# Optimization experiments

Hardware: AMD Instinct MI355X
Metric: run time of the kernel (lower is better)

## Reference

```python
import jax, jax.numpy as jnp
import numpy as np

N = 100000   # nodes
E = 1600000  # edges
IN, HID, OUT = 128, 256, 64


def _glorot(key, shape):
    fan_in, fan_out = shape[1], shape[0]
    lim = (6.0 / (fan_in + fan_out)) ** 0.5
    return jax.random.uniform(key, shape, jnp.float32, -lim, lim)


def setup_inputs() -> dict:
    key = jax.random.key(0)
    ks = jax.random.split(key, 8)
    x = jax.random.normal(ks[0], (N, IN), jnp.float32)
    edge_index = jax.random.randint(ks[1], (2, E), 0, N, jnp.int64)
    # SAGEConv params: lin_l (neighbor path, has bias), lin_r (root path, no bias)
    return {
        "x": x,
        "edge_index": edge_index,
        "W1_l": _glorot(ks[2], (HID, IN)),
        "b1": jnp.zeros((HID,), jnp.float32),
        "W1_r": _glorot(ks[3], (HID, IN)),
        "W2_l": _glorot(ks[4], (OUT, HID)),
        "b2": jnp.zeros((OUT,), jnp.float32),
        "W2_r": _glorot(ks[5], (OUT, HID)),
    }


def _sage_conv(x, src, dst, W_l, b, W_r):
    # mean aggregation of neighbor features at destination nodes
    msg = x[src]                                             # [E, d] gather
    agg = jax.ops.segment_sum(msg, dst, num_segments=N)      # [N, d]
    cnt = jax.ops.segment_sum(jnp.ones((src.shape[0],), jnp.float32), dst,
                              num_segments=N)                # [N]
    mean = agg / jnp.maximum(cnt, 1.0)[:, None]
    return mean @ W_l.T + b + x @ W_r.T


def reference(x, edge_index, W1_l, b1, W1_r, W2_l, b2, W2_r):
    src, dst = edge_index[0], edge_index[1]
    h = jax.nn.relu(_sage_conv(x, src, dst, W1_l, b1, W1_r))
    # dropout is identity in eval mode
    return _sage_conv(h, src, dst, W2_l, b2, W2_r)
```

## Files before the change

### kernel.cpp

```cpp
#include <hip/hip_runtime.h>
#include <hip/hip_bf16.h>

#define NNODE 100000
#define NEDGE 1600000
#define NBBLK 512
#define CHUNK (NEDGE / NBBLK)
#define NBUCK ((NNODE + 511) >> 9)
#define XB ((NNODE * 32 + 255) / 256)
#define WB 384

typedef __attribute__((ext_vector_type(8))) short bf16x8;
typedef __attribute__((ext_vector_type(4))) float f32x4;
typedef __attribute__((ext_vector_type(2))) float f32x2;

__device__ __forceinline__ unsigned short f2bf(float f){
  unsigned u = __float_as_uint(f);
  u += 0x7fffu + ((u >> 16) & 1u);
  return (unsigned short)(u >> 16);
}
__device__ __forceinline__ unsigned pk2(float a, float b){
  return (unsigned)f2bf(a) | ((unsigned)f2bf(b) << 16);
}
__device__ __forceinline__ float bflo(unsigned v){ return __uint_as_float(v << 16); }
__device__ __forceinline__ float bfhi(unsigned v){ return __uint_as_float(v & 0xffff0000u); }

__global__ __launch_bounds__(256) void k_xh(const float* __restrict__ x,
                                            unsigned* __restrict__ A1u,
                                            unsigned* __restrict__ x8u,
                                            const int* __restrict__ dst,
                                            unsigned* __restrict__ gh,
                                            const float* __restrict__ W1l,
                                            const float* __restrict__ W1r,
                                            const float* __restrict__ W2l,
                                            const float* __restrict__ W2r,
                                            unsigned short* __restrict__ Bwt1,
                                            unsigned short* __restrict__ Bwt2){
  int bid = blockIdx.x;
  if (bid < NBBLK){
    __shared__ unsigned h[NBUCK];
    for (int t = threadIdx.x; t < NBUCK; t += 256) h[t] = 0;
    __syncthreads();
    int base = bid * CHUNK;
    for (int j = threadIdx.x; j < CHUNK; j += 256)
      atomicAdd(&h[dst[base + j] >> 9], 1u);
    __syncthreads();
    for (int t = threadIdx.x; t < NBUCK; t += 256) gh[bid * NBUCK + t] = h[t];
    return;
  }
  if (bid < NBBLK + XB){
    int i = (bid - NBBLK) * 256 + threadIdx.x;
    if (i >= NNODE * 32) return;
    float4 v = ((const float4*)x)[i];
    int e = i * 4;
    int row = e >> 7, c = e & 127;
    unsigned* d = A1u + (size_t)row * 128 + 64 + (c >> 1);
    d[0] = pk2(v.x, v.y);
    d[1] = pk2(v.z, v.w);
    unsigned p = (unsigned)__builtin_amdgcn_cvt_pk_fp8_f32(v.x, v.y, 0, false);
    p = (unsigned)__builtin_amdgcn_cvt_pk_fp8_f32(v.z, v.w, (int)p, true);
    x8u[(size_t)row * 32 + (c >> 2)] = p;
    return;
  }
  int i = (bid - NBBLK - XB) * 256 + threadIdx.x;
  if (i < 256 * 256){
    int n = i >> 8, k = i & 255;
    float v = (k < 128) ? W1l[n * 128 + k] : W1r[n * 128 + (k - 128)];
    Bwt1[i] = f2bf(v);
  } else if (i < 256 * 256 + 128 * 256){
    int i2 = i - 256 * 256;
    int n = i2 >> 8, k = i2 & 255;
    float v = (n < 64) ? W2l[n * 256 + k] : W2r[(n - 64) * 256 + k];
    Bwt2[i2] = f2bf(v);
  }
}

__global__ __launch_bounds__(512) void k_scan512(const unsigned* __restrict__ gh,
                                                 unsigned* __restrict__ gbase,
                                                 unsigned* __restrict__ btot){
  int b = blockIdx.x, t = threadIdx.x;
  int lane = t & 63, wv = t >> 6;
  unsigned v = gh[t * NBUCK + b];
  unsigned s = v;
  #pragma unroll
  for (int off = 1; off < 64; off <<= 1){
    unsigned u = __shfl_up(s, off, 64);
    if (lane >= off) s += u;
  }
  __shared__ unsigned wsum[8];
  if (lane == 63) wsum[wv] = s;
  __syncthreads();
  unsigned woff = 0;
  for (int w = 0; w < wv; ++w) woff += wsum[w];
  gbase[t * NBUCK + b] = woff + s - v;
  if (t == 511) btot[b] = woff + s;
}

__global__ __launch_bounds__(256) void k_binscat(const int* __restrict__ src,
                                                 const int* __restrict__ dst,
                                                 const unsigned* __restrict__ gbase,
                                                 const unsigned* __restrict__ btot,
                                                 unsigned* __restrict__ pairs){
  __shared__ unsigned sb[256];
  __shared__ unsigned cur[NBUCK];
  int t = threadIdx.x;
  unsigned v = (t < NBUCK) ? btot[t] : 0u;
  sb[t] = v;
  __syncthreads();
  #pragma unroll
  for (int off = 1; off < 256; off <<= 1){
    unsigned u = (t >= off) ? sb[t - off] : 0u;
    __syncthreads();
    sb[t] += u;
    __syncthreads();
  }
  if (t < NBUCK) cur[t] = (sb[t] - v) + gbase[blockIdx.x * NBUCK + t];
  __syncthreads();
  int base = blockIdx.x * CHUNK;
  for (int j = t; j < CHUNK; j += 256){
    int s = src[base + j], d = dst[base + j];
    unsigned p = atomicAdd(&cur[d >> 9], 1u);
    pairs[p] = ((unsigned)s << 9) | (unsigned)(d & 511);
  }
}

__global__ __launch_bounds__(512) void k_buildcsr(const unsigned* __restrict__ btot,
                                                  const unsigned* __restrict__ pairs,
                                                  unsigned* __restrict__ rowptr,
                                                  unsigned* __restrict__ col){
  __shared__ unsigned sb[256];
  __shared__ unsigned hist[512];
  __shared__ unsigned wsum[8];
  __shared__ unsigned se0, se1;
  const int b = blockIdx.x, tid = threadIdx.x;
  const int lane = tid & 63, wv = tid >> 6;
  if (tid < 256){
    unsigned v = (tid < NBUCK) ? btot[tid] : 0u;
    sb[tid] = v;
  }
  __syncthreads();
  #pragma unroll
  for (int off = 1; off < 256; off <<= 1){
    unsigned u = 0;
    if (tid < 256 && tid >= off) u = sb[tid - off];
    __syncthreads();
    if (tid < 256) sb[tid] += u;
    __syncthreads();
  }
  if (tid == 0){
    se1 = sb[b];
    se0 = sb[b] - btot[b];
    if (b == 0) rowptr[NNODE] = NEDGE;
  }
  hist[tid] = 0;
  __syncthreads();
  const unsigned e0 = se0, e1 = se1;
  const int nb0 = b << 9;
  for (unsigned j = e0 + tid; j < e1; j += 512)
    atomicAdd(&hist[pairs[j] & 511u], 1u);
  __syncthreads();
  unsigned v = hist[tid];
  unsigned s = v;
  #pragma unroll
  for (int off = 1; off < 64; off <<= 1){
    unsigned u = __shfl_up(s, off, 64);
    if (lane >= off) s += u;
  }
  if (lane == 63) wsum[wv] = s;
  __syncthreads();
  unsigned woff = 0;
  for (int w = 0; w < wv; ++w) woff += wsum[w];
  unsigned gpos = e0 + woff + s - v;
  if (nb0 + tid < NNODE) rowptr[nb0 + tid] = gpos;
  __syncthreads();
  hist[tid] = gpos;
  __syncthreads();
  for (unsigned j = e0 + tid; j < e1; j += 512){
    unsigned e = pairs[j];
    unsigned p = atomicAdd(&hist[e & 511u], 1u);
    col[p] = e >> 9;
  }
}

__global__ __launch_bounds__(256) void k_agg1(const unsigned* __restrict__ rowptr,
                                              const unsigned* __restrict__ col,
                                              const unsigned* __restrict__ x8u,
                                              unsigned* __restrict__ A1u){
  int gw = (blockIdx.x * 256 + threadIdx.x) >> 6;
  int lane = threadIdx.x & 63;
  if (gw >= NNODE) return;
  unsigned s0 = rowptr[gw], s1 = rowptr[gw + 1];
  const int sel = lane >> 4, u = lane & 15;
  const uint2* x82 = (const uint2*)x8u;
  float a0=0.f,a1=0.f,a2=0.f,a3=0.f,a4=0.f,a5=0.f,a6=0.f,a7=0.f;
  f32x2 p;
  unsigned j = s0;
  for (; j + 15 < s1; j += 16){
    unsigned ca = col[j + sel], cb = col[j + 4 + sel];
    unsigned cc = col[j + 8 + sel], cd = col[j + 12 + sel];
    uint2 va = x82[(size_t)ca * 16 + u];
    uint2 vb = x82[(size_t)cb * 16 + u];
    uint2 vc = x82[(size_t)cc * 16 + u];
    uint2 vd = x82[(size_t)cd * 16 + u];
    p = __builtin_amdgcn_cvt_pk_f32_fp8((int)va.x, false); a0+=p.x; a1+=p.y;
    p = __builtin_amdgcn_cvt_pk_f32_fp8((int)va.x, true ); a2+=p.x; a3+=p.y;
    p = __builtin_amdgcn_cvt_pk_f32_fp8((int)va.y, false); a4+=p.x; a5+=p.y;
    p = __builtin_amdgcn_cvt_pk_f32_fp8((int)va.y, true ); a6+=p.x; a7+=p.y;
    p = __builtin_amdgcn_cvt_pk_f32_fp8((int)vb.x, false); a0+=p.x; a1+=p.y;
    p = __builtin_amdgcn_cvt_pk_f32_fp8((int)vb.x, true ); a2+=p.x; a3+=p.y;
    p = __builtin_amdgcn_cvt_pk_f32_fp8((int)vb.y, false); a4+=p.x; a5+=p.y;
    p = __builtin_amdgcn_cvt_pk_f32_fp8((int)vb.y, true ); a6+=p.x; a7+=p.y;
    p = __builtin_amdgcn_cvt_pk_f32_fp8((int)vc.x, false); a0+=p.x; a1+=p.y;
    p = __builtin_amdgcn_cvt_pk_f32_fp8((int)vc.x, true ); a2+=p.x; a3+=p.y;
    p = __builtin_amdgcn_cvt_pk_f32_fp8((int)vc.y, false); a4+=p.x; a5+=p.y;
    p = __builtin_amdgcn_cvt_pk_f32_fp8((int)vc.y, true ); a6+=p.x; a7+=p.y;
    p = __builtin_amdgcn_cvt_pk_f32_fp8((int)vd.x, false); a0+=p.x; a1+=p.y;
    p = __builtin_amdgcn_cvt_pk_f32_fp8((int)vd.x, true ); a2+=p.x; a3+=p.y;
    p = __builtin_amdgcn_cvt_pk_f32_fp8((int)vd.y, false); a4+=p.x; a5+=p.y;
    p = __builtin_amdgcn_cvt_pk_f32_fp8((int)vd.y, true ); a6+=p.x; a7+=p.y;
  }
  for (; j + 3 < s1; j += 4){
    unsigned ca = col[j + sel];
    uint2 va = x82[(size_t)ca * 16 + u];
    p = __builtin_amdgcn_cvt_pk_f32_fp8((int)va.x, false); a0+=p.x; a1+=p.y;
    p = __builtin_amdgcn_cvt_pk_f32_fp8((int)va.x, true ); a2+=p.x; a3+=p.y;
    p = __builtin_amdgcn_cvt_pk_f32_fp8((int)va.y, false); a4+=p.x; a5+=p.y;
    p = __builtin_amdgcn_cvt_pk_f32_fp8((int)va.y, true ); a6+=p.x; a7+=p.y;
  }
  int rem = (int)(s1 - j);
  if (sel < rem){
    unsigned ca = col[j + sel];
    uint2 va = x82[(size_t)ca * 16 + u];
    p = __builtin_amdgcn_cvt_pk_f32_fp8((int)va.x, false); a0+=p.x; a1+=p.y;
    p = __builtin_amdgcn_cvt_pk_f32_fp8((int)va.x, true ); a2+=p.x; a3+=p.y;
    p = __builtin_amdgcn_cvt_pk_f32_fp8((int)va.y, false); a4+=p.x; a5+=p.y;
    p = __builtin_amdgcn_cvt_pk_f32_fp8((int)va.y, true ); a6+=p.x; a7+=p.y;
  }
  a0 += __shfl_xor(a0, 16, 64); a1 += __shfl_xor(a1, 16, 64);
  a2 += __shfl_xor(a2, 16, 64); a3 += __shfl_xor(a3, 16, 64);
  a4 += __shfl_xor(a4, 16, 64); a5 += __shfl_xor(a5, 16, 64);
  a6 += __shfl_xor(a6, 16, 64); a7 += __shfl_xor(a7, 16, 64);
  a0 += __shfl_xor(a0, 32, 64); a1 += __shfl_xor(a1, 32, 64);
  a2 += __shfl_xor(a2, 32, 64); a3 += __shfl_xor(a3, 32, 64);
  a4 += __shfl_xor(a4, 32, 64); a5 += __shfl_xor(a5, 32, 64);
  a6 += __shfl_xor(a6, 32, 64); a7 += __shfl_xor(a7, 32, 64);
  if (lane < 16){
    float inv = 1.f / fmaxf((float)(s1 - s0), 1.f);
    uint4 w;
    w.x = pk2(a0 * inv, a1 * inv);
    w.y = pk2(a2 * inv, a3 * inv);
    w.z = pk2(a4 * inv, a5 * inv);
    w.w = pk2(a6 * inv, a7 * inv);
    *(uint4*)(A1u + (size_t)gw * 128 + 4 * lane) = w;
  }
}

template<int BN, bool RELU, bool BIAS, int MODE>
__global__ __launch_bounds__(512) void k_gemm(const unsigned short* __restrict__ A,
                                              const unsigned short* __restrict__ B,
                                              const float* __restrict__ bias,
                                              unsigned short* __restrict__ C,
                                              unsigned char* __restrict__ z8,
                                              unsigned short* __restrict__ r16,
                                              int nrows){
  constexpr int NF = BN / 64;
  __shared__ unsigned short a_t[128 * 64];
  __shared__ unsigned short b_t[BN * 64];
  const int tid = threadIdx.x, wave = tid >> 6, lane = tid & 63;
  const int wr = wave >> 2, wc = wave & 3;
  const int row0 = blockIdx.x * 128;
  char* ab = (char*)a_t;
  char* bb = (char*)b_t;

  f32x4 acc[4][NF];
  #pragma unroll
  for (int m = 0; m < 4; ++m)
    #pragma unroll
    for (int n = 0; n < NF; ++n)
      acc[m][n] = (f32x4){0.f, 0.f, 0.f, 0.f};

  for (int kt = 0; kt < 4; ++kt){
    {
      int r = tid >> 2;
      int gr = row0 + r; if (gr > nrows - 1) gr = nrows - 1;
      const uint4* s4 = (const uint4*)(A + (size_t)gr * 256 + kt * 64);
      int c0 = (tid & 3) * 2;
      uint4 v0 = s4[c0], v1 = s4[c0 + 1];
      *(uint4*)(ab + r * 128 + ((c0 * 16) ^ ((r & 7) << 4))) = v0;
      *(uint4*)(ab + r * 128 + (((c0 + 1) * 16) ^ ((r & 7) << 4))) = v1;
    }
    {
      constexpr int CPT = BN / 64;
      #pragma unroll
      for (int c = 0; c < CPT; ++c){
        int gc = tid * CPT + c;
        int n = gc >> 3, ck = gc & 7;
        uint4 v = ((const uint4*)(B + (size_t)n * 256 + kt * 64))[ck];
        *(uint4*)(bb + n * 128 + ((ck * 16) ^ ((n & 7) << 4))) = v;
      }
    }
    __syncthreads();
    #pragma unroll
    for (int kk = 0; kk < 2; ++kk){
      int k2 = (kk * 32 + ((lane >> 4) * 8)) * 2;
      bf16x8 af[4];
      #pragma unroll
      for (int m = 0; m < 4; ++m){
        int rr = wr * 64 + m * 16 + (lane & 15);
        af[m] = *(const bf16x8*)(ab + rr * 128 + (k2 ^ ((rr & 7) << 4)));
      }
      #pragma unroll
      for (int n = 0; n < NF; ++n){
        int cc = wc * (16 * NF) + n * 16 + (lane & 15);
        bf16x8 bfv = *(const bf16x8*)(bb + cc * 128 + (k2 ^ ((cc & 7) << 4)));
        #pragma unroll
        for (int m = 0; m < 4; ++m)
          acc[m][n] = __builtin_amdgcn_mfma_f32_16x16x32_bf16(af[m], bfv, acc[m][n], 0, 0, 0);
      }
    }
    __syncthreads();
  }
  #pragma unroll
  for (int m = 0; m < 4; ++m){
    int rbase = row0 + wr * 64 + m * 16 + ((lane >> 4) << 2);
    #pragma unroll
    for (int r = 0; r < 4; ++r){
      if (rbase + r < nrows){
        #pragma unroll
        for (int n = 0; n < NF; ++n){
          int cc = wc * (16 * NF) + n * 16 + (lane & 15);
          float v = acc[m][n][r];
          if (BIAS) v += bias[cc];
          if (RELU) v = fmaxf(v, 0.f);
          if (MODE == 0){
            C[(size_t)(rbase + r) * BN + cc] = f2bf(v);
          } else {
            if (cc < 64)
              z8[(size_t)(rbase + r) * 64 + cc] =
                (unsigned char)__builtin_amdgcn_cvt_pk_fp8_f32(v, v, 0, false);
            else
              r16[(size_t)(rbase + r) * 64 + (cc - 64)] = f2bf(v);
          }
        }
      }
    }
  }
}

__global__ __launch_bounds__(256) void k_agg2(const unsigned* __restrict__ rowptr,
                                              const unsigned* __restrict__ col,
                                              const unsigned* __restrict__ z8u,
                                              const unsigned* __restrict__ r16u,
                                              const float* __restrict__ b2,
                                              float* __restrict__ out){
  int gw = (blockIdx.x * 256 + threadIdx.x) >> 6;
  int lane = threadIdx.x & 63;
  if (gw >= NNODE) return;
  unsigned s0 = rowptr[gw], s1 = rowptr[gw + 1];
  const int sel = lane >> 4, u = lane & 15;
  float a0=0.f,a1=0.f,a2=0.f,a3=0.f;
  f32x2 p;
  unsigned j = s0;
  for (; j + 15 < s1; j += 16){
    unsigned ca = col[j + sel], cb = col[j + 4 + sel];
    unsigned cc = col[j + 8 + sel], cd = col[j + 12 + sel];
    unsigned va = z8u[(size_t)ca * 16 + u];
    unsigned vb = z8u[(size_t)cb * 16 + u];
    unsigned vc = z8u[(size_t)cc * 16 + u];
    unsigned vd = z8u[(size_t)cd * 16 + u];
    p = __builtin_amdgcn_cvt_pk_f32_fp8((int)va, false); a0+=p.x; a1+=p.y;
    p = __builtin_amdgcn_cvt_pk_f32_fp8((int)va, true ); a2+=p.x; a3+=p.y;
    p = __builtin_amdgcn_cvt_pk_f32_fp8((int)vb, false); a0+=p.x; a1+=p.y;
    p = __builtin_amdgcn_cvt_pk_f32_fp8((int)vb, true ); a2+=p.x; a3+=p.y;
    p = __builtin_amdgcn_cvt_pk_f32_fp8((int)vc, false); a0+=p.x; a1+=p.y;
    p = __builtin_amdgcn_cvt_pk_f32_fp8((int)vc, true ); a2+=p.x; a3+=p.y;
    p = __builtin_amdgcn_cvt_pk_f32_fp8((int)vd, false); a0+=p.x; a1+=p.y;
    p = __builtin_amdgcn_cvt_pk_f32_fp8((int)vd, true ); a2+=p.x; a3+=p.y;
  }
  for (; j + 3 < s1; j += 4){
    unsigned ca = col[j + sel];
    unsigned va = z8u[(size_t)ca * 16 + u];
    p = __builtin_amdgcn_cvt_pk_f32_fp8((int)va, false); a0+=p.x; a1+=p.y;
    p = __builtin_amdgcn_cvt_pk_f32_fp8((int)va, true ); a2+=p.x; a3+=p.y;
  }
  int rem = (int)(s1 - j);
  if (sel < rem){
    unsigned ca = col[j + sel];
    unsigned va = z8u[(size_t)ca * 16 + u];
    p = __builtin_amdgcn_cvt_pk_f32_fp8((int)va, false); a0+=p.x; a1+=p.y;
    p = __builtin_amdgcn_cvt_pk_f32_fp8((int)va, true ); a2+=p.x; a3+=p.y;
  }
  a0 += __shfl_xor(a0, 16, 64); a1 += __shfl_xor(a1, 16, 64);
  a2 += __shfl_xor(a2, 16, 64); a3 += __shfl_xor(a3, 16, 64);
  a0 += __shfl_xor(a0, 32, 64); a1 += __shfl_xor(a1, 32, 64);
  a2 += __shfl_xor(a2, 32, 64); a3 += __shfl_xor(a3, 32, 64);
  if (lane < 16){
    float inv = 1.f / fmaxf((float)(s1 - s0), 1.f);
    uint2 rv = ((const uint2*)(r16u + (size_t)gw * 32))[lane];
    float4 bv = ((const float4*)b2)[lane];
    float4 res;
    res.x = a0 * inv + bflo(rv.x) + bv.x;
    res.y = a1 * inv + bfhi(rv.x) + bv.y;
    res.z = a2 * inv + bflo(rv.y) + bv.z;
    res.w = a3 * inv + bfhi(rv.y) + bv.w;
    ((float4*)out)[(size_t)gw * 16 + lane] = res;
  }
}

extern "C" void kernel_launch(void* const* d_in, const int* in_sizes, int n_in,
                              void* d_out, int out_size, void* d_ws, size_t ws_size,
                              hipStream_t stream) {
  const float* x   = (const float*)d_in[0];
  const int*   ei  = (const int*)d_in[1];
  const float* W1l = (const float*)d_in[2];
  const float* b1  = (const float*)d_in[3];
  const float* W1r = (const float*)d_in[4];
  const float* W2l = (const float*)d_in[5];
  const float* b2  = (const float*)d_in[6];
  const float* W2r = (const float*)d_in[7];
  float* out = (float*)d_out;

  char* ws = (char*)d_ws;
  size_t off = 0;
  auto alloc = [&](size_t bytes) -> void* {
    void* p = ws + off;
    off = (off + bytes + 255) & ~(size_t)255;
    return p;
  };
  unsigned* rowptr = (unsigned*)alloc((size_t)(NNODE + 1) * 4);
  unsigned* col    = (unsigned*)alloc((size_t)NEDGE * 4);
  unsigned* pairs  = (unsigned*)alloc((size_t)NEDGE * 4);
  unsigned* gh     = (unsigned*)alloc((size_t)NBBLK * NBUCK * 4);
  unsigned* gbase  = (unsigned*)alloc((size_t)NBBLK * NBUCK * 4);
  unsigned* btot   = (unsigned*)alloc((size_t)NBUCK * 4);
  unsigned short* A1   = (unsigned short*)alloc((size_t)NNODE * 256 * 2);
  unsigned short* h    = (unsigned short*)alloc((size_t)NNODE * 256 * 2);
  unsigned short* r16  = (unsigned short*)alloc((size_t)NNODE * 64 * 2);
  unsigned* x8u        = (unsigned*)alloc((size_t)NNODE * 32 * 4);
  unsigned char* z8    = (unsigned char*)alloc((size_t)NNODE * 64);
  unsigned short* Bwt1 = (unsigned short*)alloc(256 * 256 * 2);
  unsigned short* Bwt2 = (unsigned short*)alloc(128 * 256 * 2);

  const int* srcv = ei;
  const int* dstv = ei + NEDGE;

  k_xh<<<NBBLK + XB + WB, 256, 0, stream>>>(x, (unsigned*)A1, x8u, dstv, gh,
                                            W1l, W1r, W2l, W2r, Bwt1, Bwt2);
  k_scan512<<<NBUCK, 512, 0, stream>>>(gh, gbase, btot);
  k_binscat<<<NBBLK, 256, 0, stream>>>(srcv, dstv, gbase, btot, pairs);
  k_buildcsr<<<NBUCK, 512, 0, stream>>>(btot, pairs, rowptr, col);

  k_agg1<<<(NNODE + 3) / 4, 256, 0, stream>>>(rowptr, col, x8u, (unsigned*)A1);

  int gblocks = (NNODE + 127) / 128;
  k_gemm<256, true,  true,  0><<<gblocks, 512, 0, stream>>>(A1, Bwt1, b1, h, nullptr, nullptr, NNODE);
  k_gemm<128, false, false, 2><<<gblocks, 512, 0, stream>>>(h,  Bwt2, nullptr, nullptr, z8, r16, NNODE);

  k_agg2<<<(NNODE + 3) / 4, 256, 0, stream>>>(rowptr, col, (const unsigned*)z8, (const unsigned*)r16, b2, out);
}
```

Baseline: 297.2 us.

## Fuse the two dense GEMMs so hidden activations stay in shared memory

The layer-1 GEMM (bias, ReLU) and the layer-2 GEMM now run in one kernel. Each block writes its 128x256 hidden tile as bf16 into swizzled shared memory and immediately multiplies it by the second weight matrix. This removes the global write and re-read of the N x 256 bf16 hidden tensor plus one kernel launch. In exchange the kernel uses 64 KB of LDS, which cuts occupancy, and it holds more accumulators in registers. The x conversion kernel also packs its two bf16 words into a single 8-byte store.

```diff
diff --git a/kernel.cpp b/kernel.cpp
--- a/kernel.cpp
+++ b/kernel.cpp
@@ -53,9 +53,10 @@
     float4 v = ((const float4*)x)[i];
     int e = i * 4;
     int row = e >> 7, c = e & 127;
-    unsigned* d = A1u + (size_t)row * 128 + 64 + (c >> 1);
-    d[0] = pk2(v.x, v.y);
-    d[1] = pk2(v.z, v.w);
+    uint2 w;
+    w.x = pk2(v.x, v.y);
+    w.y = pk2(v.z, v.w);
+    *(uint2*)(A1u + (size_t)row * 128 + 64 + (c >> 1)) = w;
     unsigned p = (unsigned)__builtin_amdgcn_cvt_pk_fp8_f32(v.x, v.y, 0, false);
     p = (unsigned)__builtin_amdgcn_cvt_pk_fp8_f32(v.z, v.w, (int)p, true);
     x8u[(size_t)row * 32 + (c >> 2)] = p;
@@ -254,29 +255,28 @@
   }
 }
 
-template<int BN, bool RELU, bool BIAS, int MODE>
-__global__ __launch_bounds__(512) void k_gemm(const unsigned short* __restrict__ A,
-                                              const unsigned short* __restrict__ B,
-                                              const float* __restrict__ bias,
-                                              unsigned short* __restrict__ C,
-                                              unsigned char* __restrict__ z8,
-                                              unsigned short* __restrict__ r16,
-                                              int nrows){
-  constexpr int NF = BN / 64;
-  __shared__ unsigned short a_t[128 * 64];
-  __shared__ unsigned short b_t[BN * 64];
+__global__ __launch_bounds__(512) void k_gemmf(const unsigned short* __restrict__ A,
+                                               const unsigned short* __restrict__ B1,
+                                               const float* __restrict__ bias1,
+                                               const unsigned short* __restrict__ B2,
+                                               unsigned char* __restrict__ z8,
+                                               unsigned short* __restrict__ r16,
+                                               int nrows){
+  __shared__ char smem[65536];
+  char* ab  = smem;
+  char* bb  = smem + 16384;
+  char* hb  = smem;
+  char* bb2 = smem + 32768;
   const int tid = threadIdx.x, wave = tid >> 6, lane = tid & 63;
   const int wr = wave >> 2, wc = wave & 3;
   const int row0 = blockIdx.x * 128;
-  char* ab = (char*)a_t;
-  char* bb = (char*)b_t;
-
-  f32x4 acc[4][NF];
+
+  f32x4 acc1[4][4];
   #pragma unroll
   for (int m = 0; m < 4; ++m)
     #pragma unroll
-    for (int n = 0; n < NF; ++n)
-      acc[m][n] = (f32x4){0.f, 0.f, 0.f, 0.f};
+    for (int n = 0; n < 4; ++n)
+      acc1[m][n] = (f32x4){0.f, 0.f, 0.f, 0.f};
 
   for (int kt = 0; kt < 4; ++kt){
     {
@@ -289,12 +289,11 @@
       *(uint4*)(ab + r * 128 + (((c0 + 1) * 16) ^ ((r & 7) << 4))) = v1;
     }
     {
-      constexpr int CPT = BN / 64;
-      #pragma unroll
-      for (int c = 0; c < CPT; ++c){
-        int gc = tid * CPT + c;
+      #pragma unroll
+      for (int c = 0; c < 4; ++c){
+        int gc = tid * 4 + c;
         int n = gc >> 3, ck = gc & 7;
-        uint4 v = ((const uint4*)(B + (size_t)n * 256 + kt * 64))[ck];
+        uint4 v = ((const uint4*)(B1 + (size_t)n * 256 + kt * 64))[ck];
         *(uint4*)(bb + n * 128 + ((ck * 16) ^ ((n & 7) << 4))) = v;
       }
     }
@@ -309,16 +308,78 @@
         af[m] = *(const bf16x8*)(ab + rr * 128 + (k2 ^ ((rr & 7) << 4)));
       }
       #pragma unroll
-      for (int n = 0; n < NF; ++n){
-        int cc = wc * (16 * NF) + n * 16 + (lane & 15);
+      for (int n = 0; n < 4; ++n){
+        int cc = wc * 64 + n * 16 + (lane & 15);
         bf16x8 bfv = *(const bf16x8*)(bb + cc * 128 + (k2 ^ ((cc & 7) << 4)));
         #pragma unroll
         for (int m = 0; m < 4; ++m)
-          acc[m][n] = __builtin_amdgcn_mfma_f32_16x16x32_bf16(af[m], bfv, acc[m][n], 0, 0, 0);
-      }
-    }
-    __syncthreads();
-  }
+          acc1[m][n] = __builtin_amdgcn_mfma_f32_16x16x32_bf16(af[m], bfv, acc1[m][n], 0, 0, 0);
+      }
+    }
+    __syncthreads();
+  }
+
+  float bv[4];
+  #pragma unroll
+  for (int n = 0; n < 4; ++n) bv[n] = bias1[wc * 64 + n * 16 + (lane & 15)];
+
+  f32x4 acc2[4][2];
+  #pragma unroll
+  for (int m = 0; m < 4; ++m)
+    #pragma unroll
+    for (int n = 0; n < 2; ++n)
+      acc2[m][n] = (f32x4){0.f, 0.f, 0.f, 0.f};
+
+  for (int kh = 0; kh < 2; ++kh){
+    {
+      #pragma unroll
+      for (int c = 0; c < 4; ++c){
+        int gc = tid * 4 + c;
+        int n = gc >> 4, ck = gc & 15;
+        uint4 v = ((const uint4*)(B2 + (size_t)n * 256 + kh * 128))[ck];
+        *(uint4*)(bb2 + n * 256 + ((ck * 16) ^ ((n & 7) << 4)));
+        *(uint4*)(bb2 + n * 256 + ((ck * 16) ^ ((n & 7) << 4))) = v;
+      }
+    }
+    if ((wc >> 1) == kh){
+      #pragma unroll
+      for (int m = 0; m < 4; ++m){
+        int row = wr * 64 + m * 16 + ((lane >> 4) << 2);
+        #pragma unroll
+        for (int r = 0; r < 4; ++r){
+          int rw = row + r;
+          #pragma unroll
+          for (int n = 0; n < 4; ++n){
+            int cl = (wc & 1) * 64 + n * 16 + (lane & 15);
+            float v = fmaxf(acc1[m][n][r] + bv[n], 0.f);
+            int byte = rw * 256 + (((cl >> 3) * 16) ^ ((rw & 7) << 4)) + (cl & 7) * 2;
+            *(unsigned short*)(hb + byte) = f2bf(v);
+          }
+        }
+      }
+    }
+    __syncthreads();
+    #pragma unroll
+    for (int kk = 0; kk < 4; ++kk){
+      int k2 = (kk * 32 + ((lane >> 4) * 8)) * 2;
+      bf16x8 af[4];
+      #pragma unroll
+      for (int m = 0; m < 4; ++m){
+        int rr = wr * 64 + m * 16 + (lane & 15);
+        af[m] = *(const bf16x8*)(hb + rr * 256 + (k2 ^ ((rr & 7) << 4)));
+      }
+      #pragma unroll
+      for (int n = 0; n < 2; ++n){
+        int cc = wc * 32 + n * 16 + (lane & 15);
+        bf16x8 bfv = *(const bf16x8*)(bb2 + cc * 256 + (k2 ^ ((cc & 7) << 4)));
+        #pragma unroll
+        for (int m = 0; m < 4; ++m)
+          acc2[m][n] = __builtin_amdgcn_mfma_f32_16x16x32_bf16(af[m], bfv, acc2[m][n], 0, 0, 0);
+      }
+    }
+    __syncthreads();
+  }
+
   #pragma unroll
   for (int m = 0; m < 4; ++m){
     int rbase = row0 + wr * 64 + m * 16 + ((lane >> 4) << 2);
@@ -326,20 +387,14 @@
     for (int r = 0; r < 4; ++r){
       if (rbase + r < nrows){
         #pragma unroll
-        for (int n = 0; n < NF; ++n){
-          int cc = wc * (16 * NF) + n * 16 + (lane & 15);
-          float v = acc[m][n][r];
-          if (BIAS) v += bias[cc];
-          if (RELU) v = fmaxf(v, 0.f);
-          if (MODE == 0){
-            C[(size_t)(rbase + r) * BN + cc] = f2bf(v);
-          } else {
-            if (cc < 64)
-              z8[(size_t)(rbase + r) * 64 + cc] =
-                (unsigned char)__builtin_amdgcn_cvt_pk_fp8_f32(v, v, 0, false);
-            else
-              r16[(size_t)(rbase + r) * 64 + (cc - 64)] = f2bf(v);
-          }
+        for (int n = 0; n < 2; ++n){
+          int cc = wc * 32 + n * 16 + (lane & 15);
+          float v = acc2[m][n][r];
+          if (cc < 64)
+            z8[(size_t)(rbase + r) * 64 + cc] =
+              (unsigned char)__builtin_amdgcn_cvt_pk_fp8_f32(v, v, 0, false);
+          else
+            r16[(size_t)(rbase + r) * 64 + (cc - 64)] = f2bf(v);
         }
       }
     }
@@ -433,7 +488,6 @@
   unsigned* gbase  = (unsigned*)alloc((size_t)NBBLK * NBUCK * 4);
   unsigned* btot   = (unsigned*)alloc((size_t)NBUCK * 4);
   unsigned short* A1   = (unsigned short*)alloc((size_t)NNODE * 256 * 2);
-  unsigned short* h    = (unsigned short*)alloc((size_t)NNODE * 256 * 2);
   unsigned short* r16  = (unsigned short*)alloc((size_t)NNODE * 64 * 2);
   unsigned* x8u        = (unsigned*)alloc((size_t)NNODE * 32 * 4);
   unsigned char* z8    = (unsigned char*)alloc((size_t)NNODE * 64);
@@ -452,8 +506,7 @@
   k_agg1<<<(NNODE + 3) / 4, 256, 0, stream>>>(rowptr, col, x8u, (unsigned*)A1);
 
   int gblocks = (NNODE + 127) / 128;
-  k_gemm<256, true,  true,  0><<<gblocks, 512, 0, stream>>>(A1, Bwt1, b1, h, nullptr, nullptr, NNODE);
-  k_gemm<128, false, false, 2><<<gblocks, 512, 0, stream>>>(h,  Bwt2, nullptr, nullptr, z8, r16, NNODE);
+  k_gemmf<<<gblocks, 512, 0, stream>>>(A1, Bwt1, b1, Bwt2, z8, r16, NNODE);
 
   k_agg2<<<(NNODE + 3) / 4, 256, 0, stream>>>(rowptr, col, (const unsigned*)z8, (const unsigned*)r16, b2, out);
 }
```

After: 292.8 us. About the same (-1.5%).
